# Kernel optimization log

Measured on AMD Instinct MI355X. Metric: run time of the kernel, lower is better.

The kernel has to match this reference:

```python
import jax, jax.numpy as jnp
import numpy as np

B, S, D_IN, D_K, D_OUT = 8, 2048, 1024, 64, 64

def setup_inputs() -> dict:
    key = jax.random.key(0)
    k1, k2, k3, k4 = jax.random.split(key, 4)
    sc = 1.0 / np.sqrt(D_IN)
    return {
        "X": jax.random.normal(k1, (B, S, D_IN), dtype=jnp.float32),
        "Wq": jax.random.normal(k2, (D_IN, D_K), dtype=jnp.float32) * sc,
        "Wk": jax.random.normal(k3, (D_IN, D_K), dtype=jnp.float32) * sc,
        "Wv": jax.random.normal(k4, (D_IN, D_OUT), dtype=jnp.float32) * sc,
    }

def reference(X, Wq, Wk, Wv):
    # projections (no bias)
    Q = jnp.einsum('bsd,dk->bsk', X, Wq)   # [B,S,d_k]
    K = jnp.einsum('bsd,dk->bsk', X, Wk)   # [B,S,d_k]
    V = jnp.einsum('bsd,dv->bsv', X, Wv)   # [B,S,d_out]
    d_k = Q.shape[-1]
    S_mat = jnp.einsum('bqk,bsk->bqs', Q, K) / jnp.sqrt(jnp.float32(d_k))
    # causal mask: positions j > i get -inf
    causal = jnp.tril(jnp.ones((X.shape[1], X.shape[1]), dtype=bool))
    S_mat = jnp.where(causal[None, :, :], S_mat, -jnp.inf)
    A = jax.nn.softmax(S_mat, axis=-1)
    return jnp.einsum('bqs,bsv->bqv', A, V)
```

## Files before the change

### kernel.cpp

```cpp
#include <hip/hip_runtime.h>
#include <hip/hip_bf16.h>
#include <cstdint>
#include <cstddef>

#define BATCH 8
#define SEQ   2048
#define DIN   1024

typedef float f32x4 __attribute__((ext_vector_type(4)));
typedef float f32x8 __attribute__((ext_vector_type(8)));
typedef __bf16 bf16x4 __attribute__((ext_vector_type(4)));
typedef __bf16 bf16x8 __attribute__((ext_vector_type(8)));
typedef unsigned short ushort8_t __attribute__((ext_vector_type(8)));

__device__ __forceinline__ unsigned short bfu(float f) {
  __bf16 h = (__bf16)f;
  return __builtin_bit_cast(unsigned short, h);
}

__device__ __forceinline__ bf16x8 cvt8pair(float4 a, float4 b) {
  f32x8 v;
  v[0] = a.x; v[1] = a.y; v[2] = a.z; v[3] = a.w;
  v[4] = b.x; v[5] = b.y; v[6] = b.z; v[7] = b.w;
  return __builtin_convertvector(v, bf16x8);
}

__global__ void pack_w(const float* __restrict__ Wq, const float* __restrict__ Wk,
                       const float* __restrict__ Wv, unsigned short* __restrict__ Wp) {
  const int t = blockIdx.x * blockDim.x + threadIdx.x;
  const int lane = t & 63;
  const int grp = t >> 6;
  const int ks = grp & 31;
  const int nt = grp >> 5;
  const int n = nt * 16 + (lane & 15);
  const int k0 = ks * 32 + ((lane >> 4) << 3);
  const float* W;
  int col;
  float scale = 1.0f;
  if (n < 64)       { W = Wq; col = n;       scale = 0.18033688011112042f; }
  else if (n < 128) { W = Wk; col = n - 64;  }
  else              { W = Wv; col = n - 128; }
  ushort8_t out;
#pragma unroll
  for (int j = 0; j < 8; ++j)
    out[j] = bfu(W[(size_t)(k0 + j) * 64 + col] * scale);
  reinterpret_cast<ushort8_t*>(Wp)[t] = out;
}

__global__ __launch_bounds__(256, 2) void qkv_gemm(
    const float* __restrict__ X, const unsigned short* __restrict__ Wp,
    unsigned short* __restrict__ Qb, unsigned short* __restrict__ Kf,
    unsigned short* __restrict__ Vf) {
  __shared__ ushort8_t Af[2][2048];

  const int tid = threadIdx.x;
  const int lane = tid & 63;
  const int wave = tid >> 6;
  const int l15 = lane & 15;
  const int quad = lane >> 4;
  const int m0 = blockIdx.x * 32;
  const int nt0 = wave * 3;

  const int sr = tid >> 3;
  const int sk = tid & 7;
  const float* xrow = X + (size_t)(m0 + sr) * DIN;

  const ushort8_t* wp = reinterpret_cast<const ushort8_t*>(Wp) + nt0 * 2048 + lane;
  ushort8_t breg[2][3];
#pragma unroll
  for (int p = 0; p < 2; ++p)
#pragma unroll
    for (int nt = 0; nt < 3; ++nt) breg[p][nt] = wp[p * 64 + nt * 2048];

  f32x4 acc[2][3];
#pragma unroll
  for (int mt = 0; mt < 2; ++mt)
#pragma unroll
    for (int nt = 0; nt < 3; ++nt) acc[mt][nt] = (f32x4){0.f, 0.f, 0.f, 0.f};

  auto compute_half = [&](int ksbase, const ushort8_t* A) {
    ushort8_t a0 = A[quad * 32 + l15];
    ushort8_t a1 = A[quad * 32 + 16 + l15];
    for (int ksl = 0; ksl < 16; ++ksl) {
      const int ks = ksbase + ksl;
      const int p = ks & 1;
      bf16x8 af0 = __builtin_bit_cast(bf16x8, a0);
      bf16x8 af1 = __builtin_bit_cast(bf16x8, a1);
      bf16x8 b0 = __builtin_bit_cast(bf16x8, breg[p][0]);
      bf16x8 b1 = __builtin_bit_cast(bf16x8, breg[p][1]);
      bf16x8 b2 = __builtin_bit_cast(bf16x8, breg[p][2]);
      if (ksl < 15) {
        a0 = A[((ksl + 1) * 4 + quad) * 32 + l15];
        a1 = A[((ksl + 1) * 4 + quad) * 32 + 16 + l15];
      }
      if (ks < 30) {
#pragma unroll
        for (int nt = 0; nt < 3; ++nt)
          breg[p][nt] = wp[(ks + 2) * 64 + nt * 2048];
      }
      acc[0][0] = __builtin_amdgcn_mfma_f32_16x16x32_bf16(af0, b0, acc[0][0], 0, 0, 0);
      acc[0][1] = __builtin_amdgcn_mfma_f32_16x16x32_bf16(af0, b1, acc[0][1], 0, 0, 0);
      acc[0][2] = __builtin_amdgcn_mfma_f32_16x16x32_bf16(af0, b2, acc[0][2], 0, 0, 0);
      acc[1][0] = __builtin_amdgcn_mfma_f32_16x16x32_bf16(af1, b0, acc[1][0], 0, 0, 0);
      acc[1][1] = __builtin_amdgcn_mfma_f32_16x16x32_bf16(af1, b1, acc[1][1], 0, 0, 0);
      acc[1][2] = __builtin_amdgcn_mfma_f32_16x16x32_bf16(af1, b2, acc[1][2], 0, 0, 0);
    }
  };

  float4 xbuf[16];
#pragma unroll
  for (int p = 0; p < 2; ++p) {
    const float4* src = reinterpret_cast<const float4*>(xrow + (sk + p * 8) * 32);
#pragma unroll
    for (int i = 0; i < 8; ++i) xbuf[p * 8 + i] = src[i];
  }
#pragma unroll
  for (int p = 0; p < 2; ++p) {
    const int ksl = sk + p * 8;
#pragma unroll
    for (int q = 0; q < 4; ++q)
      Af[0][(ksl * 4 + q) * 32 + sr] =
          __builtin_bit_cast(ushort8_t, cvt8pair(xbuf[p * 8 + q * 2], xbuf[p * 8 + q * 2 + 1]));
  }
  __syncthreads();

#pragma unroll
  for (int p = 0; p < 2; ++p) {
    const float4* src = reinterpret_cast<const float4*>(xrow + (16 + sk + p * 8) * 32);
#pragma unroll
    for (int i = 0; i < 8; ++i) xbuf[p * 8 + i] = src[i];
  }

  compute_half(0, Af[0]);

#pragma unroll
  for (int p = 0; p < 2; ++p) {
    const int ksl = sk + p * 8;
#pragma unroll
    for (int q = 0; q < 4; ++q)
      Af[1][(ksl * 4 + q) * 32 + sr] =
          __builtin_bit_cast(ushort8_t, cvt8pair(xbuf[p * 8 + q * 2], xbuf[p * 8 + q * 2 + 1]));
  }
  __syncthreads();

  compute_half(16, Af[1]);

#pragma unroll
  for (int mt = 0; mt < 2; ++mt) {
    const int srow = m0 + mt * 16 + quad * 4;
    const int b = srow >> 11;
    const int s = srow & 2047;
#pragma unroll
    for (int nt = 0; nt < 3; ++nt) {
      const f32x4 a = acc[mt][nt];
      const int n = (nt0 + nt) * 16 + l15;
      if (n < 64) {
#pragma unroll
        for (int r = 0; r < 4; ++r)
          Qb[(size_t)(srow + r) * 64 + n] = bfu(a[r]);
      } else if (n < 128) {
        const int dk = n - 64;
        const int dh = dk >> 5, kq = (dk >> 3) & 3, kj = dk & 7;
        const int kt = s >> 6, hh = (s >> 4) & 3;
        unsigned short* kdst = Kf + (((size_t)(b * 32 + kt) * 8 + hh * 2 + dh) << 9)
                                  + (kq * 16 + quad * 4) * 8 + kj;
#pragma unroll
        for (int r = 0; r < 4; ++r) kdst[r * 8] = bfu(a[r]);
      } else {
        const int dv = n - 128;
        const int vnt = dv >> 4, vl = dv & 15;
        const int kt = s >> 6, vc = (s >> 5) & 1, vq = (s >> 3) & 3, j0 = s & 7;
        ushort4 t4;
        t4.x = bfu(a[0]); t4.y = bfu(a[1]);
        t4.z = bfu(a[2]); t4.w = bfu(a[3]);
        *reinterpret_cast<ushort4*>(Vf + (((size_t)(b * 32 + kt) * 8 + vc * 4 + vnt) << 9)
                                       + (vq * 16 + vl) * 8 + j0) = t4;
      }
    }
  }
}

__global__ __launch_bounds__(256, 2) void flash_kernel(
    const unsigned short* __restrict__ Qb, const unsigned short* __restrict__ Kf,
    const unsigned short* __restrict__ Vf, float* __restrict__ Out) {
  __shared__ float Olds[4][2][16][68];
  __shared__ float Llds[4][2][16];
  __shared__ __attribute__((aligned(16))) unsigned short Pf[4][2][2][512];

  const int tid = threadIdx.x;
  const int lane = tid & 63;
  const int wave = tid >> 6;
  const int l15 = lane & 15;
  const int quad = lane >> 4;

  const int g = blockIdx.x;
  const int batch = g & 7;
  const int jj = (g >> 3) & 31;
  const int qb = (g < 256) ? (63 - jj) : jj;
  const int q0 = qb * 32;
  const int n64 = (q0 + 95) >> 6;

  bf16x8 qf[2][2];
#pragma unroll
  for (int mt = 0; mt < 2; ++mt) {
    const ushort8_t* qp = reinterpret_cast<const ushort8_t*>(
        Qb + (size_t)(batch * SEQ + q0 + mt * 16 + l15) * 64);
    qf[mt][0] = __builtin_bit_cast(bf16x8, qp[quad]);
    qf[mt][1] = __builtin_bit_cast(bf16x8, qp[4 + quad]);
  }

  const ushort8_t* kfb = reinterpret_cast<const ushort8_t*>(Kf)
                         + (size_t)batch * 32 * 512 + lane;
  const ushort8_t* vfb = reinterpret_cast<const ushort8_t*>(Vf)
                         + (size_t)batch * 32 * 512 + lane;

  const int pbase = l15 * 8 + (quad >> 1) * 128 + (quad & 1) * 4;

  f32x4 o[2][4];
  float lacc[2];
#pragma unroll
  for (int mt = 0; mt < 2; ++mt) {
    lacc[mt] = 0.f;
#pragma unroll
    for (int i = 0; i < 4; ++i) o[mt][i] = (f32x4){0.f, 0.f, 0.f, 0.f};
  }

  ushort8_t kbuf[8], vbuf[8];
  if (wave < n64) {
    const ushort8_t* kp = kfb + wave * 512;
#pragma unroll
    for (int i = 0; i < 8; ++i) kbuf[i] = kp[i * 64];
    const ushort8_t* vp = vfb + wave * 512;
#pragma unroll
    for (int i = 0; i < 8; ++i) vbuf[i] = vp[i * 64];
  }

  for (int kt = wave; kt < n64; kt += 4) {
    const int k0 = kt * 64;
    const int nk = (kt + 4 < n64) ? kt + 4 : n64 - 1;
    f32x4 s[2][4];
    __builtin_amdgcn_s_setprio(1);
#pragma unroll
    for (int h = 0; h < 4; ++h) {
      bf16x8 kf0 = __builtin_bit_cast(bf16x8, kbuf[h * 2]);
      bf16x8 kf1 = __builtin_bit_cast(bf16x8, kbuf[h * 2 + 1]);
#pragma unroll
      for (int mt = 0; mt < 2; ++mt) {
        f32x4 z = (f32x4){0.f, 0.f, 0.f, 0.f};
        z = __builtin_amdgcn_mfma_f32_16x16x32_bf16(kf0, qf[mt][0], z, 0, 0, 0);
        z = __builtin_amdgcn_mfma_f32_16x16x32_bf16(kf1, qf[mt][1], z, 0, 0, 0);
        s[mt][h] = z;
      }
    }
    __builtin_amdgcn_s_setprio(0);
    {
      const ushort8_t* kp = kfb + nk * 512;
#pragma unroll
      for (int i = 0; i < 8; ++i) kbuf[i] = kp[i * 64];
    }
    if (kt == n64 - 1) {
#pragma unroll
      for (int mt = 0; mt < 2; ++mt) {
        const int row = q0 + mt * 16 + l15;
#pragma unroll
        for (int h = 0; h < 4; ++h) {
          const int colb = k0 + h * 16 + quad * 4;
#pragma unroll
          for (int r = 0; r < 4; ++r)
            if (colb + r > row) s[mt][h][r] = -INFINITY;
        }
      }
    }
#pragma unroll
    for (int mt = 0; mt < 2; ++mt) {
#pragma unroll
      for (int h = 0; h < 4; ++h) {
        f32x4 p;
#pragma unroll
        for (int r = 0; r < 4; ++r) p[r] = __builtin_amdgcn_exp2f(s[mt][h][r]);
        lacc[mt] += (p[0] + p[1]) + (p[2] + p[3]);
        bf16x4 pk = __builtin_convertvector(p, bf16x4);
        *reinterpret_cast<unsigned long long*>(
            &Pf[wave][mt][h >> 1][pbase + ((h & 1) << 8)]) =
            __builtin_bit_cast(unsigned long long, pk);
      }
    }
#pragma unroll
    for (int c = 0; c < 2; ++c) {
      bf16x8 pfm[2];
#pragma unroll
      for (int mt = 0; mt < 2; ++mt)
        pfm[mt] = __builtin_bit_cast(bf16x8,
            reinterpret_cast<const ushort8_t*>(&Pf[wave][mt][c][0])[lane]);
      __builtin_amdgcn_s_setprio(1);
#pragma unroll
      for (int nt = 0; nt < 4; ++nt) {
        bf16x8 vf = __builtin_bit_cast(bf16x8, vbuf[c * 4 + nt]);
#pragma unroll
        for (int mt = 0; mt < 2; ++mt)
          o[mt][nt] = __builtin_amdgcn_mfma_f32_16x16x32_bf16(pfm[mt], vf, o[mt][nt], 0, 0, 0);
      }
      __builtin_amdgcn_s_setprio(0);
    }
    {
      const ushort8_t* vp = vfb + nk * 512;
#pragma unroll
      for (int i = 0; i < 8; ++i) vbuf[i] = vp[i * 64];
    }
  }

#pragma unroll
  for (int off = 16; off < 64; off <<= 1)
#pragma unroll
    for (int mt = 0; mt < 2; ++mt)
      lacc[mt] += __shfl_xor(lacc[mt], off, 64);

#pragma unroll
  for (int mt = 0; mt < 2; ++mt) {
#pragma unroll
    for (int nt = 0; nt < 4; ++nt)
#pragma unroll
      for (int r = 0; r < 4; ++r)
        Olds[wave][mt][quad * 4 + r][nt * 16 + l15] = o[mt][nt][r];
    if (quad == 0) Llds[wave][mt][l15] = lacc[mt];
  }
  __syncthreads();

  const int col = tid & 63;
  const int r0 = tid >> 6;
#pragma unroll
  for (int row = r0; row < 32; row += 4) {
    const int mt = row >> 4;
    const int rr = row & 15;
    float lstar = 0.f, accv = 0.f;
#pragma unroll
    for (int w = 0; w < 4; ++w) {
      lstar += Llds[w][mt][rr];
      accv += Olds[w][mt][rr][col];
    }
    Out[(size_t)(batch * SEQ + q0 + row) * 64 + col] = accv / lstar;
  }
}

extern "C" void kernel_launch(void* const* d_in, const int* in_sizes, int n_in,
                              void* d_out, int out_size, void* d_ws, size_t ws_size,
                              hipStream_t stream) {
  const float* X  = (const float*)d_in[0];
  const float* Wq = (const float*)d_in[1];
  const float* Wk = (const float*)d_in[2];
  const float* Wv = (const float*)d_in[3];
  float* Out = (float*)d_out;

  char* ws = (char*)d_ws;
  unsigned short* Wp = (unsigned short*)ws;
  unsigned short* Qb = (unsigned short*)(ws + (400 << 10));
  unsigned short* Kf = (unsigned short*)(ws + (400 << 10) + (2 << 20));
  unsigned short* Vf = (unsigned short*)(ws + (400 << 10) + (4 << 20));

  pack_w<<<96, 256, 0, stream>>>(Wq, Wk, Wv, Wp);
  qkv_gemm<<<512, 256, 0, stream>>>(X, Wp, Qb, Kf, Vf);
  flash_kernel<<<512, 256, 0, stream>>>(Qb, Kf, Vf, Out);
}
```

Baseline: 122.5 us.

## Software-pipeline attention loop so PV of previous tile overlaps exp of current

```diff
diff --git a/kernel.cpp b/kernel.cpp
--- a/kernel.cpp
+++ b/kernel.cpp
@@ -226,19 +226,21 @@
   }
 
   ushort8_t kbuf[8], vbuf[8];
-  if (wave < n64) {
-    const ushort8_t* kp = kfb + wave * 512;
+  f32x4 s[2][4];
+  unsigned long long pk[2][4];
+  bf16x8 pfm[2][2];
+
+  auto load_k = [&](int t) {
+    const ushort8_t* kp = kfb + t * 512;
 #pragma unroll
     for (int i = 0; i < 8; ++i) kbuf[i] = kp[i * 64];
-    const ushort8_t* vp = vfb + wave * 512;
+  };
+  auto load_v = [&](int t) {
+    const ushort8_t* vp = vfb + t * 512;
 #pragma unroll
     for (int i = 0; i < 8; ++i) vbuf[i] = vp[i * 64];
-  }
-
-  for (int kt = wave; kt < n64; kt += 4) {
-    const int k0 = kt * 64;
-    const int nk = (kt + 4 < n64) ? kt + 4 : n64 - 1;
-    f32x4 s[2][4];
+  };
+  auto do_qk = [&]() {
     __builtin_amdgcn_s_setprio(1);
 #pragma unroll
     for (int h = 0; h < 4; ++h) {
@@ -253,12 +255,10 @@
       }
     }
     __builtin_amdgcn_s_setprio(0);
-    {
-      const ushort8_t* kp = kfb + nk * 512;
-#pragma unroll
-      for (int i = 0; i < 8; ++i) kbuf[i] = kp[i * 64];
-    }
+  };
+  auto do_exp = [&](int kt) {
     if (kt == n64 - 1) {
+      const int k0 = kt * 64;
 #pragma unroll
       for (int mt = 0; mt < 2; ++mt) {
         const int row = q0 + mt * 16 + l15;
@@ -272,41 +272,65 @@
       }
     }
 #pragma unroll
-    for (int mt = 0; mt < 2; ++mt) {
+    for (int mt = 0; mt < 2; ++mt)
 #pragma unroll
       for (int h = 0; h < 4; ++h) {
         f32x4 p;
 #pragma unroll
         for (int r = 0; r < 4; ++r) p[r] = __builtin_amdgcn_exp2f(s[mt][h][r]);
         lacc[mt] += (p[0] + p[1]) + (p[2] + p[3]);
-        bf16x4 pk = __builtin_convertvector(p, bf16x4);
+        pk[mt][h] =
+            __builtin_bit_cast(unsigned long long, __builtin_convertvector(p, bf16x4));
+      }
+  };
+  auto write_p = [&]() {
+#pragma unroll
+    for (int mt = 0; mt < 2; ++mt)
+#pragma unroll
+      for (int h = 0; h < 4; ++h)
         *reinterpret_cast<unsigned long long*>(
-            &Pf[wave][mt][h >> 1][pbase + ((h & 1) << 8)]) =
-            __builtin_bit_cast(unsigned long long, pk);
-      }
-    }
-#pragma unroll
-    for (int c = 0; c < 2; ++c) {
-      bf16x8 pfm[2];
-#pragma unroll
-      for (int mt = 0; mt < 2; ++mt)
-        pfm[mt] = __builtin_bit_cast(bf16x8,
+            &Pf[wave][mt][h >> 1][pbase + ((h & 1) << 8)]) = pk[mt][h];
+  };
+  auto read_pfm = [&]() {
+#pragma unroll
+    for (int mt = 0; mt < 2; ++mt)
+#pragma unroll
+      for (int c = 0; c < 2; ++c)
+        pfm[mt][c] = __builtin_bit_cast(bf16x8,
             reinterpret_cast<const ushort8_t*>(&Pf[wave][mt][c][0])[lane]);
-      __builtin_amdgcn_s_setprio(1);
+  };
+  auto do_pv = [&]() {
+    __builtin_amdgcn_s_setprio(1);
+#pragma unroll
+    for (int c = 0; c < 2; ++c)
 #pragma unroll
       for (int nt = 0; nt < 4; ++nt) {
         bf16x8 vf = __builtin_bit_cast(bf16x8, vbuf[c * 4 + nt]);
 #pragma unroll
         for (int mt = 0; mt < 2; ++mt)
-          o[mt][nt] = __builtin_amdgcn_mfma_f32_16x16x32_bf16(pfm[mt], vf, o[mt][nt], 0, 0, 0);
-      }
-      __builtin_amdgcn_s_setprio(0);
-    }
-    {
-      const ushort8_t* vp = vfb + nk * 512;
-#pragma unroll
-      for (int i = 0; i < 8; ++i) vbuf[i] = vp[i * 64];
-    }
+          o[mt][nt] = __builtin_amdgcn_mfma_f32_16x16x32_bf16(pfm[mt][c], vf, o[mt][nt], 0, 0, 0);
+      }
+    __builtin_amdgcn_s_setprio(0);
+  };
+
+  if (wave < n64) {
+    load_k(wave);
+    load_v(wave);
+    do_qk();
+    load_k((wave + 4 < n64) ? wave + 4 : n64 - 1);
+    do_exp(wave);
+    write_p();
+    for (int kt = wave + 4; kt < n64; kt += 4) {
+      do_qk();
+      load_k((kt + 4 < n64) ? kt + 4 : n64 - 1);
+      read_pfm();
+      do_exp(kt);
+      do_pv();
+      write_p();
+      load_v(kt);
+    }
+    read_pfm();
+    do_pv();
   }
 
 #pragma unroll
```

Result: no change. 123.0 us (+0.4%).
